# Kernel tuning notes

Measured on AMD Instinct MI355X. Metric: run time of the kernel, lower is better.

## Reference

```python
import jax, jax.numpy as jnp
import numpy as np

N_TRAIN = 16384
B_TEST = 4096
M_HALF = 768                 # modes per side -> M = 2*m+1 quadrature nodes
M_NODES = 2 * M_HALF + 1     # 1537
L_FFT = 4 * M_HALF + 1       # circulant embedding length (= 2*M-1)
H_SPACING = 0.01
SIGMASQ = 0.1
ELL = 0.1                    # SE kernel lengthscale
PROBES = 64
STEPS = 50
CG_ITERS = 50
TWO_PI = 2.0 * np.pi
EVAL_FLOOR = 1e-18


def setup_inputs():
    key = jax.random.key(0)
    k1, k2, k3, k4 = jax.random.split(key, 4)
    x = jax.random.uniform(k1, (N_TRAIN, 1), dtype=jnp.float32)
    y = jax.random.normal(k2, (N_TRAIN,), dtype=jnp.float32)
    x_new = jax.random.uniform(k3, (B_TEST, 1), dtype=jnp.float32)
    z = jax.random.normal(k4, (PROBES, M_NODES), dtype=jnp.float32)
    return {"x": x, "y": y, "x_new": x_new, "z": z}


def _cg(Aop, b, iters):
    """Conjugate gradients on Hermitian PD system, fixed iteration count."""
    x0 = jnp.zeros_like(b)
    rs0 = jnp.real(jnp.vdot(b, b))
    def step(carry, _):
        xk, rk, pk, rs = carry
        Ap = Aop(pk)
        a = (rs / jnp.real(jnp.vdot(pk, Ap))).astype(b.dtype)
        xk = xk + a * pk
        rk = rk - a * Ap
        rs_new = jnp.real(jnp.vdot(rk, rk))
        pk = rk + (rs_new / rs).astype(b.dtype) * pk
        return (xk, rk, pk, rs_new), None
    (xk, _, _, _), _ = jax.lax.scan(step, (x0, b, b, rs0), None, length=iters)
    return xk


def _efgp_forward(x, y, x_new, z):
    m = M_HALF
    ks = jnp.arange(-m, m + 1, dtype=jnp.float32)           # (M,)
    xis = H_SPACING * ks
    # squared-exponential spectral density, unit variance
    S = np.sqrt(TWO_PI) * ELL * jnp.exp(-2.0 * (np.pi * ELL * xis) ** 2)
    ws = jnp.sqrt(H_SPACING * S).astype(jnp.complex64)      # (M,) quadrature weights

    xf = x[:, 0]
    # convolution vector v[p] = sum_n exp(2*pi*i*h*p*x_n), p in [-2m, 2m]
    ps = jnp.arange(-2 * m, 2 * m + 1, dtype=jnp.float32)   # (L,)
    phase_v = (TWO_PI * H_SPACING) * jnp.outer(xf, ps)      # (N, L)
    vfull = jnp.exp(1j * phase_v).sum(axis=0)               # (L,) complex64
    # circulant first column c[q] = t[q] = v[-q]; T[j,k] = v[k-j]
    c = jnp.roll(vfull[::-1], 2 * m + 1)
    c_fft = jnp.fft.fft(c)

    def toeplitz(u):  # u: (..., M) complex -> (..., M)
        pad = jnp.zeros(u.shape[:-1] + (L_FFT - M_NODES,), u.dtype)
        upad = jnp.concatenate([u, pad], axis=-1)
        return jnp.fft.ifft(jnp.fft.fft(upad, axis=-1) * c_fft, axis=-1)[..., :M_NODES]

    # Fourier feature matrix F[n,k] = exp(2*pi*i*h*k*x_n)
    F = jnp.exp(1j * (TWO_PI * H_SPACING) * jnp.outer(xf, ks))  # (N, M)
    yc = y.astype(jnp.complex64)
    rhs = ws * (F.conj().T @ yc)                                 # ws * F^H y

    def A_mean(beta):  # ws T ws beta + sigma^2 beta
        return ws * toeplitz(ws * beta) + SIGMASQ * beta

    beta = _cg(A_mean, rhs, CG_ITERS)

    Fn = jnp.exp(1j * (TWO_PI * H_SPACING) * jnp.outer(x_new[:, 0], ks))  # (B, M)
    mean = jnp.real(Fn @ (ws * beta))                                      # (B,)

    # ---- stochastic Lanczos quadrature log-det of I + sigma^-2 D T D ----
    def Av(v):
        return v + (1.0 / SIGMASQ) * (ws * toeplitz(ws * v))

    zr = jnp.sign(z).astype(jnp.complex64)  # Rademacher probes (P, M)

    def lanczos(z1):
        nz2 = jnp.real(jnp.vdot(z1, z1))
        q0 = z1 / jnp.sqrt(nz2)
        def step(carry, _):
            q, q_prev, beta_prev = carry
            v = Av(q) - beta_prev * q_prev
            alpha = jnp.real(jnp.vdot(q, v))
            v = v - alpha * q
            beta = jnp.sqrt(jnp.real(jnp.vdot(v, v)))
            q_new = v / jnp.maximum(beta, 1e-12)
            return (q_new, q, beta), (alpha, beta)
        init = (q0, jnp.zeros_like(q0), jnp.zeros((), jnp.float32))
        _, (alphas, betas) = jax.lax.scan(step, init, None, length=STEPS)
        return alphas, betas, nz2

    alphas, betas, nz2 = jax.vmap(lanczos)(zr)  # (P, STEPS)

    def tridiag(a, b):
        return jnp.diag(a) + jnp.diag(b[:-1], 1) + jnp.diag(b[:-1], -1)

    Ts = jax.vmap(tridiag)(alphas, betas)       # (P, STEPS, STEPS)
    evals, evecs = jnp.linalg.eigh(Ts)
    evals = jnp.maximum(evals, EVAL_FLOOR)
    w1 = evecs[:, 0, :]                         # first component of each Ritz vector
    quad = jnp.sum(w1 ** 2 * jnp.log(evals), axis=-1) * nz2  # (P,)
    logdet = jnp.mean(quad) + N_TRAIN * np.log(SIGMASQ)

    alpha_vec = jnp.real(yc - F @ (ws * beta)) / SIGMASQ
    lml = -0.5 * jnp.dot(y, alpha_vec) - 0.5 * logdet \
          - 0.5 * N_TRAIN * np.log(2.0 * np.pi)
    return mean, lml


def reference(x, y, x_new, z):
    return _efgp_forward(x, y, x_new, z)
```

## Files before the change

kernel.cpp:

```cpp
#include <hip/hip_runtime.h>
#include <hip/hip_cooperative_groups.h>
#include <math.h>

namespace cg = cooperative_groups;

#define MN 1537
#define NFFT 4096
#define FBN (NFFT + NFFT/8 + NFFT/64)
#define CW 0.06283185307179587f
#define W4096 1.5339807878856412e-3f

__device__ __forceinline__ float2 cmulf(float2 a, float2 b) {
    return make_float2(a.x*b.x - a.y*b.y, a.x*b.y + a.y*b.x);
}
__device__ __forceinline__ float2 cadd(float2 a, float2 b){ return make_float2(a.x+b.x, a.y+b.y); }
__device__ __forceinline__ float2 csub(float2 a, float2 b){ return make_float2(a.x-b.x, a.y-b.y); }
__device__ __forceinline__ float2 mulnegi(float2 z){ return make_float2(z.y, -z.x); }
__device__ __forceinline__ float2 mulposi(float2 z){ return make_float2(-z.y, z.x); }
__device__ __forceinline__ float2 cconj(float2 z){ return make_float2(z.x, -z.y); }
__device__ __forceinline__ int PHI(int i){ return i + (i >> 3) + (i >> 6); }

__device__ __forceinline__ float ws_at(int k) {
    float xi = 0.01f * (float)(k - 768);
    float t  = 0.31415926535897931f * xi;
    float S  = 0.25066282746310002f * expf(-2.0f * t * t);
    return sqrtf(0.01f * S);
}

struct Tw { float2 w1, w2, w4, c1, c3; };

__device__ __forceinline__ Tw make_tw(float ang){
    Tw t;
    __sincosf(ang, &t.w1.y, &t.w1.x);
    t.w2 = cmulf(t.w1, t.w1);
    t.w4 = cmulf(t.w2, t.w2);
    const float R = 0.70710678118654752f;
    t.c1 = cmulf(t.w1, make_float2( R, -R));
    t.c3 = cmulf(t.w1, make_float2(-R, -R));
    return t;
}

template<int S>
__device__ __forceinline__ void fwd8c(float2* fb, int tt, const Tw& w){
    const int Q = 1 << (S-2);
    const int p = tt & (Q-1);
    const int g = tt >> (S-2);
    const int base = (g << (S+1)) + p;
    float2 a0 = fb[PHI(base      )], a1 = fb[PHI(base +   Q)];
    float2 a2 = fb[PHI(base + 2*Q)], a3 = fb[PHI(base + 3*Q)];
    float2 a4 = fb[PHI(base + 4*Q)], a5 = fb[PHI(base + 5*Q)];
    float2 a6 = fb[PHI(base + 6*Q)], a7 = fb[PHI(base + 7*Q)];
    float2 b0 = cadd(a0,a4), b1 = cadd(a1,a5), b2 = cadd(a2,a6), b3 = cadd(a3,a7);
    float2 b4 = cmulf(csub(a0,a4), w.w1);
    float2 b5 = cmulf(csub(a1,a5), w.c1);
    float2 b6 = mulnegi(cmulf(csub(a2,a6), w.w1));
    float2 b7 = cmulf(csub(a3,a7), w.c3);
    float2 c0 = cadd(b0,b2), c2 = cmulf(csub(b0,b2), w.w2);
    float2 c1 = cadd(b1,b3), c3 = mulnegi(cmulf(csub(b1,b3), w.w2));
    float2 c4 = cadd(b4,b6), c6 = cmulf(csub(b4,b6), w.w2);
    float2 c5 = cadd(b5,b7), c7 = mulnegi(cmulf(csub(b5,b7), w.w2));
    fb[PHI(base      )] = cadd(c0,c1);
    fb[PHI(base +   Q)] = cmulf(csub(c0,c1), w.w4);
    fb[PHI(base + 2*Q)] = cadd(c2,c3);
    fb[PHI(base + 3*Q)] = cmulf(csub(c2,c3), w.w4);
    fb[PHI(base + 4*Q)] = cadd(c4,c5);
    fb[PHI(base + 5*Q)] = cmulf(csub(c4,c5), w.w4);
    fb[PHI(base + 6*Q)] = cadd(c6,c7);
    fb[PHI(base + 7*Q)] = cmulf(csub(c6,c7), w.w4);
}

template<int S>
__device__ __forceinline__ void inv8c(float2* fb, int tt, const Tw& w){
    const int Q = 1 << S;
    const int p = tt & (Q-1);
    const int g = tt >> S;
    const int base = (g << (S+3)) + p;
    float2 u1 = cconj(w.w1), u2 = cconj(w.w2), u4 = cconj(w.w4);
    float2 uc1 = cconj(w.c1), uc3 = cconj(w.c3);
    float2 a0 = fb[PHI(base      )], a1 = fb[PHI(base +   Q)];
    float2 a2 = fb[PHI(base + 2*Q)], a3 = fb[PHI(base + 3*Q)];
    float2 a4 = fb[PHI(base + 4*Q)], a5 = fb[PHI(base + 5*Q)];
    float2 a6 = fb[PHI(base + 6*Q)], a7 = fb[PHI(base + 7*Q)];
    float2 m;
    m = cmulf(a1, u4); float2 t0 = cadd(a0,m), t1 = csub(a0,m);
    m = cmulf(a3, u4); float2 t2 = cadd(a2,m), t3 = csub(a2,m);
    m = cmulf(a5, u4); float2 t4 = cadd(a4,m), t5 = csub(a4,m);
    m = cmulf(a7, u4); float2 t6 = cadd(a6,m), t7 = csub(a6,m);
    m = cmulf(t2, u2);          float2 e0 = cadd(t0,m), e2 = csub(t0,m);
    m = mulposi(cmulf(t3, u2)); float2 e1 = cadd(t1,m), e3 = csub(t1,m);
    m = cmulf(t6, u2);          float2 e4 = cadd(t4,m), e6 = csub(t4,m);
    m = mulposi(cmulf(t7, u2)); float2 e5 = cadd(t5,m), e7 = csub(t5,m);
    m = cmulf(e4, u1);          fb[PHI(base      )] = cadd(e0,m); fb[PHI(base + 4*Q)] = csub(e0,m);
    m = cmulf(e5, uc1);         fb[PHI(base +   Q)] = cadd(e1,m); fb[PHI(base + 5*Q)] = csub(e1,m);
    m = mulposi(cmulf(e6, u1)); fb[PHI(base + 2*Q)] = cadd(e2,m); fb[PHI(base + 6*Q)] = csub(e2,m);
    m = cmulf(e7, uc3);         fb[PHI(base + 3*Q)] = cadd(e3,m); fb[PHI(base + 7*Q)] = csub(e3,m);
}

__device__ __forceinline__ void fwd8_first(float2* fb, int tt, const Tw& w, const float2* in){
    float2 b0 = in[0], b1 = in[1], b2 = in[2], b3 = in[3];
    float2 b4 = cmulf(in[0], w.w1);
    float2 b5 = cmulf(in[1], w.c1);
    float2 b6 = mulnegi(cmulf(in[2], w.w1));
    float2 b7 = cmulf(in[3], w.c3);
    float2 c0 = cadd(b0,b2), c2 = cmulf(csub(b0,b2), w.w2);
    float2 c1 = cadd(b1,b3), c3 = mulnegi(cmulf(csub(b1,b3), w.w2));
    float2 c4 = cadd(b4,b6), c6 = cmulf(csub(b4,b6), w.w2);
    float2 c5 = cadd(b5,b7), c7 = mulnegi(cmulf(csub(b5,b7), w.w2));
    fb[PHI(tt       )] = cadd(c0,c1);
    fb[PHI(tt +  512)] = cmulf(csub(c0,c1), w.w4);
    fb[PHI(tt + 1024)] = cadd(c2,c3);
    fb[PHI(tt + 1536)] = cmulf(csub(c2,c3), w.w4);
    fb[PHI(tt + 2048)] = cadd(c4,c5);
    fb[PHI(tt + 2560)] = cmulf(csub(c4,c5), w.w4);
    fb[PHI(tt + 3072)] = cadd(c6,c7);
    fb[PHI(tt + 3584)] = cmulf(csub(c6,c7), w.w4);
}

__device__ __forceinline__ void inv8_last(const float2* fb, int tt, const Tw& w, float2* outv){
    float2 u1 = cconj(w.w1), u2 = cconj(w.w2), u4 = cconj(w.w4);
    float2 uc1 = cconj(w.c1), uc3 = cconj(w.c3);
    float2 a0 = fb[PHI(tt       )], a1 = fb[PHI(tt +  512)];
    float2 a2 = fb[PHI(tt + 1024)], a3 = fb[PHI(tt + 1536)];
    float2 a4 = fb[PHI(tt + 2048)], a5 = fb[PHI(tt + 2560)];
    float2 a6 = fb[PHI(tt + 3072)], a7 = fb[PHI(tt + 3584)];
    float2 m;
    m = cmulf(a1, u4); float2 t0 = cadd(a0,m), t1 = csub(a0,m);
    m = cmulf(a3, u4); float2 t2 = cadd(a2,m), t3 = csub(a2,m);
    m = cmulf(a5, u4); float2 t4 = cadd(a4,m), t5 = csub(a4,m);
    m = cmulf(a7, u4); float2 t6 = cadd(a6,m), t7 = csub(a6,m);
    m = cmulf(t2, u2);          float2 e0 = cadd(t0,m), e2 = csub(t0,m);
    m = mulposi(cmulf(t3, u2)); float2 e1 = cadd(t1,m), e3 = csub(t1,m);
    m = cmulf(t6, u2);          float2 e4 = cadd(t4,m), e6 = csub(t4,m);
    m = mulposi(cmulf(t7, u2)); float2 e5 = cadd(t5,m), e7 = csub(t5,m);
    outv[0] = cadd(e0, cmulf(e4, u1));
    outv[1] = cadd(e1, cmulf(e5, uc1));
    outv[2] = cadd(e2, mulposi(cmulf(e6, u1)));
    outv[3] = cadd(e3, cmulf(e7, uc3));
}

__device__ __forceinline__ void mid8(float2* fb, int tt, const float2* g){
    const float R = 0.70710678118654752f;
    const int base = tt << 3;
    float2 a0 = fb[PHI(base  )], a1 = fb[PHI(base+1)];
    float2 a2 = fb[PHI(base+2)], a3 = fb[PHI(base+3)];
    float2 a4 = fb[PHI(base+4)], a5 = fb[PHI(base+5)];
    float2 a6 = fb[PHI(base+6)], a7 = fb[PHI(base+7)];
    float2 b0 = cadd(a0,a4), b1 = cadd(a1,a5), b2 = cadd(a2,a6), b3 = cadd(a3,a7);
    float2 b4 = csub(a0,a4);
    float2 b5 = cmulf(csub(a1,a5), make_float2( R, -R));
    float2 b6 = mulnegi(csub(a2,a6));
    float2 b7 = cmulf(csub(a3,a7), make_float2(-R, -R));
    float2 c0 = cadd(b0,b2), c2 = csub(b0,b2);
    float2 c1 = cadd(b1,b3), c3 = mulnegi(csub(b1,b3));
    float2 c4 = cadd(b4,b6), c6 = csub(b4,b6);
    float2 c5 = cadd(b5,b7), c7 = mulnegi(csub(b5,b7));
    float2 d0 = cadd(c0,c1), d1 = csub(c0,c1);
    float2 d2 = cadd(c2,c3), d3 = csub(c2,c3);
    float2 d4 = cadd(c4,c5), d5 = csub(c4,c5);
    float2 d6 = cadd(c6,c7), d7 = csub(c6,c7);
    d0 = cmulf(d0, g[0]); d1 = cmulf(d1, g[1]); d2 = cmulf(d2, g[2]); d3 = cmulf(d3, g[3]);
    d4 = cmulf(d4, g[4]); d5 = cmulf(d5, g[5]); d6 = cmulf(d6, g[6]); d7 = cmulf(d7, g[7]);
    float2 m;
    m = d1; float2 t0 = cadd(d0,m), t1 = csub(d0,m);
    m = d3; float2 t2 = cadd(d2,m), t3 = csub(d2,m);
    m = d5; float2 t4 = cadd(d4,m), t5 = csub(d4,m);
    m = d7; float2 t6 = cadd(d6,m), t7 = csub(d6,m);
    m = t2;          float2 e0 = cadd(t0,m), e2 = csub(t0,m);
    m = mulposi(t3); float2 e1 = cadd(t1,m), e3 = csub(t1,m);
    m = t6;          float2 e4 = cadd(t4,m), e6 = csub(t4,m);
    m = mulposi(t7); float2 e5 = cadd(t5,m), e7 = csub(t5,m);
    m = e4;                           fb[PHI(base  )] = cadd(e0,m); fb[PHI(base+4)] = csub(e0,m);
    m = cmulf(e5, make_float2(R, R)); fb[PHI(base+1)] = cadd(e1,m); fb[PHI(base+5)] = csub(e1,m);
    m = mulposi(e6);                  fb[PHI(base+2)] = cadd(e2,m); fb[PHI(base+6)] = csub(e2,m);
    m = cmulf(e7, make_float2(-R, R));fb[PHI(base+3)] = cadd(e3,m); fb[PHI(base+7)] = csub(e3,m);
}

__device__ __forceinline__ void fwd8_last_reg(const float2* fb, int tt, float2* gout){
    const float R = 0.70710678118654752f;
    const int base = tt << 3;
    float2 a0 = fb[PHI(base  )], a1 = fb[PHI(base+1)];
    float2 a2 = fb[PHI(base+2)], a3 = fb[PHI(base+3)];
    float2 a4 = fb[PHI(base+4)], a5 = fb[PHI(base+5)];
    float2 a6 = fb[PHI(base+6)], a7 = fb[PHI(base+7)];
    float2 b0 = cadd(a0,a4), b1 = cadd(a1,a5), b2 = cadd(a2,a6), b3 = cadd(a3,a7);
    float2 b4 = csub(a0,a4);
    float2 b5 = cmulf(csub(a1,a5), make_float2( R, -R));
    float2 b6 = mulnegi(csub(a2,a6));
    float2 b7 = cmulf(csub(a3,a7), make_float2(-R, -R));
    float2 c0 = cadd(b0,b2), c2 = csub(b0,b2);
    float2 c1 = cadd(b1,b3), c3 = mulnegi(csub(b1,b3));
    float2 c4 = cadd(b4,b6), c6 = csub(b4,b6);
    float2 c5 = cadd(b5,b7), c7 = mulnegi(csub(b5,b7));
    gout[0] = cadd(c0,c1); gout[1] = csub(c0,c1);
    gout[2] = cadd(c2,c3); gout[3] = csub(c2,c3);
    gout[4] = cadd(c4,c5); gout[5] = csub(c4,c5);
    gout[6] = cadd(c6,c7); gout[7] = csub(c6,c7);
}

__device__ __forceinline__ void conv_fft(float2* fb, const float2* g, int tid,
                                         const Tw& T11, const Tw& T8, const Tw& T5,
                                         const float2* in, float2* outv){
    __syncthreads();
    fwd8_first(fb, tid, T11, in); __syncthreads();
    fwd8c<8>(fb, tid, T8); __syncthreads();
    fwd8c<5>(fb, tid, T5); __syncthreads();
    mid8(fb, tid, g);      __syncthreads();
    inv8c<3>(fb, tid, T5); __syncthreads();
    inv8c<6>(fb, tid, T8); __syncthreads();
    inv8_last(fb, tid, T11, outv);
}

__device__ float block_reduce8(float v, volatile float* sc) {
    int lane = threadIdx.x & 63, wid = threadIdx.x >> 6;
    #pragma unroll
    for (int off = 32; off > 0; off >>= 1) v += __shfl_down(v, off, 64);
    if (lane == 0) sc[wid] = v;
    __syncthreads();
    if (wid == 0) {
        float s = (lane < 8) ? sc[lane] : 0.0f;
        #pragma unroll
        for (int off = 4; off > 0; off >>= 1) s += __shfl_down(s, off, 64);
        if (lane == 0) sc[16] = s;
    }
    __syncthreads();
    return sc[16];
}

__device__ float2 block_reduce2(float2 v, volatile float* sc) {
    int lane = threadIdx.x & 63, wid = threadIdx.x >> 6;
    #pragma unroll
    for (int off = 32; off > 0; off >>= 1) {
        v.x += __shfl_down(v.x, off, 64);
        v.y += __shfl_down(v.y, off, 64);
    }
    if (lane == 0) { sc[wid] = v.x; sc[17 + wid] = v.y; }
    __syncthreads();
    if (wid == 0) {
        float sx = (lane < 8) ? sc[lane] : 0.0f;
        float sy = (lane < 8) ? sc[17 + lane] : 0.0f;
        #pragma unroll
        for (int off = 4; off > 0; off >>= 1) {
            sx += __shfl_down(sx, off, 64);
            sy += __shfl_down(sy, off, 64);
        }
        if (lane == 0) { sc[16] = sx; sc[33] = sy; }
    }
    __syncthreads();
    return make_float2(sc[16], sc[33]);
}

__global__ __launch_bounds__(512) __attribute__((amdgpu_waves_per_eu(2, 2)))
void mega(const float* __restrict__ x, const float* __restrict__ y,
          const float* __restrict__ xn, const float* __restrict__ z,
          float* __restrict__ out,
          float2* __restrict__ d_v, float2* __restrict__ d_rhs, float2* __restrict__ d_wb,
          float* __restrict__ d_al, float* __restrict__ d_be, float* __restrict__ d_nz2,
          float* __restrict__ d_quad, float* __restrict__ d_t1p)
{
    __shared__ float2 fb[FBN];
    __shared__ float  redb[40];
    cg::grid_group grid = cg::this_grid();
    const int b = blockIdx.x, tid = threadIdx.x;
    const int wid = tid >> 6, lane = tid & 63;

    for (int c = b*8 + wid; c < 3073 + MN; c += 2048) {
        bool is_v = c < 3073;
        float pk = is_v ? (float)(c - 1536) : (float)(c - 3073 - 768);
        float sx = 0.f, sy = 0.f;
        if (is_v){
            for (int j = 0; j < 256; ++j){
                float ph = CW * (x[j*64 + lane] * pk);
                float s, cc; __sincosf(ph, &s, &cc);
                sx += cc; sy += s;
            }
        } else {
            for (int j = 0; j < 256; ++j){
                int n = j*64 + lane;
                float yv = y[n];
                float ph = CW * (x[n] * pk);
                float s, cc; __sincosf(ph, &s, &cc);
                sx += cc*yv; sy -= s*yv;
            }
        }
        #pragma unroll
        for (int off = 32; off > 0; off >>= 1){
            sx += __shfl_down(sx, off, 64);
            sy += __shfl_down(sy, off, 64);
        }
        if (lane == 0){
            if (is_v) d_v[c] = make_float2(sx, sy);
            else      d_rhs[c - 3073] = make_float2(sx, sy);
        }
    }
    grid.sync();

    if (b < 65) {
        Tw T11 = make_tw(-W4096 * (float)tid);
        Tw T8  = make_tw(-W4096 * (float)((tid & 63) << 3));
        Tw T5  = make_tw(-W4096 * (float)((tid & 7)  << 6));
        bool on3 = (tid == 0);
        float w[4];
        w[0] = ws_at(tid); w[1] = ws_at(tid + 512); w[2] = ws_at(tid + 1024);
        w[3] = on3 ? ws_at(1536) : 0.f;

        float2 g[8];
        #pragma unroll
        for (int k = 0; k < 8; ++k){
            int i = tid + k*512;
            float2 val = make_float2(0.f, 0.f);
            if (i == 0)            val = d_v[1536];
            else if (i <= 1536)    val = d_v[1536 - i];
            else if (i >= 2560)    val = d_v[5632 - i];
            fb[PHI(i)] = val;
        }
        __syncthreads();
        fwd8c<11>(fb, tid, T11); __syncthreads();
        fwd8c<8 >(fb, tid, T8);  __syncthreads();
        fwd8c<5 >(fb, tid, T5);  __syncthreads();
        fwd8_last_reg(fb, tid, g);

        float2 sin_[4], cv[4];
        if (b < 64) {
            float2 q[4], qp[4];
            float part = 0.f;
            #pragma unroll
            for (int s = 0; s < 4; ++s){
                float sv = 0.f;
                if (s < 3 || on3){
                    float zv = z[b*MN + tid + s*512];
                    sv = (zv > 0.f) ? 1.f : ((zv < 0.f) ? -1.f : 0.f);
                }
                q[s] = make_float2(sv, 0.f);
                qp[s] = make_float2(0.f, 0.f);
                part += sv * sv;
            }
            float nz2 = block_reduce8(part, redb);
            if (tid == 0) d_nz2[b] = nz2;
            float qs = 1.0f / sqrtf(nz2);
            #pragma unroll
            for (int s = 0; s < 4; ++s){ q[s].x *= qs; q[s].y *= qs; }
            float bp = 0.f;
            float cf[4];
            #pragma unroll
            for (int s = 0; s < 4; ++s) cf[s] = w[s] * (10.0f / 4096.0f);
            for (int step = 0; step < 50; ++step) {
                #pragma unroll
                for (int s = 0; s < 4; ++s)
                    sin_[s] = make_float2(w[s]*q[s].x, w[s]*q[s].y);
                conv_fft(fb, g, tid, T11, T8, T5, sin_, cv);
                float2 v[4];
                float2 pp = make_float2(0.f, 0.f);
                #pragma unroll
                for (int s = 0; s < 4; ++s){
                    v[s] = make_float2(q[s].x + cf[s]*cv[s].x - bp*qp[s].x,
                                       q[s].y + cf[s]*cv[s].y - bp*qp[s].y);
                    pp.x += q[s].x*v[s].x + q[s].y*v[s].y;
                    pp.y += v[s].x*v[s].x + v[s].y*v[s].y;
                }
                float2 rr = block_reduce2(pp, redb);
                float alpha = rr.x;
                float beta = sqrtf(fmaxf(rr.y - alpha*alpha, 0.f));
                if (tid == 0) { d_al[b*50 + step] = alpha; d_be[b*50 + step] = beta; }
                float binv = 1.0f / fmaxf(beta, 1e-12f);
                #pragma unroll
                for (int s = 0; s < 4; ++s){
                    float2 nq = make_float2((v[s].x - alpha*q[s].x)*binv,
                                            (v[s].y - alpha*q[s].y)*binv);
                    qp[s] = q[s];
                    q[s] = nq;
                }
                bp = beta;
            }
        } else {
            float2 r[4], p[4], xx[4];
            float part = 0.f;
            #pragma unroll
            for (int s = 0; s < 4; ++s){
                float2 bj = make_float2(0.f, 0.f);
                if (s < 3 || on3){
                    float2 rv = d_rhs[tid + s*512];
                    bj = make_float2(w[s]*rv.x, w[s]*rv.y);
                }
                r[s] = bj; p[s] = bj; xx[s] = make_float2(0.f, 0.f);
                part += bj.x*bj.x + bj.y*bj.y;
            }
            float rs = block_reduce8(part, redb);
            float cf[4];
            #pragma unroll
            for (int s = 0; s < 4; ++s) cf[s] = w[s] * (1.0f / 4096.0f);
            for (int it = 0; it < 50; ++it) {
                #pragma unroll
                for (int s = 0; s < 4; ++s)
                    sin_[s] = make_float2(w[s]*p[s].x, w[s]*p[s].y);
                conv_fft(fb, g, tid, T11, T8, T5, sin_, cv);
                float2 ap[4];
                part = 0.f;
                #pragma unroll
                for (int s = 0; s < 4; ++s){
                    ap[s] = make_float2(cf[s]*cv[s].x + 0.1f*p[s].x,
                                        cf[s]*cv[s].y + 0.1f*p[s].y);
                    part += p[s].x*ap[s].x + p[s].y*ap[s].y;
                }
                float pAp = block_reduce8(part, redb);
                float a = rs / pAp;
                part = 0.f;
                #pragma unroll
                for (int s = 0; s < 4; ++s){
                    xx[s].x += a*p[s].x; xx[s].y += a*p[s].y;
                    r[s].x -= a*ap[s].x; r[s].y -= a*ap[s].y;
                    part += r[s].x*r[s].x + r[s].y*r[s].y;
                }
                float rsn = block_reduce8(part, redb);
                float sc = rsn / rs;
                #pragma unroll
                for (int s = 0; s < 4; ++s)
                    p[s] = make_float2(r[s].x + sc*p[s].x, r[s].y + sc*p[s].y);
                rs = rsn;
            }
            #pragma unroll
            for (int s = 0; s < 4; ++s){
                if (s < 3 || on3)
                    d_wb[tid + s*512] = make_float2(w[s]*xx[s].x, w[s]*xx[s].y);
            }
        }
    }
    grid.sync();

    if (b < 64) {
        if (tid < 64) {
            float* sa  = (float*)fb;
            float* se  = sa + 64;
            float* se2 = sa + 128;
            int t = tid;
            if (t < 50) {
                sa[t] = d_al[b*50 + t];
                float bv = (t < 49) ? d_be[b*50 + t] : 0.0f;
                se[t] = bv; se2[t] = bv * bv;
            }
            float quad = 0.0f;
            if (t < 50) {
                float lo = 3.4e38f, hi = -3.4e38f;
                for (int i = 0; i < 50; ++i) {
                    float rr = ((i > 0) ? fabsf(se[i-1]) : 0.0f) + ((i < 49) ? fabsf(se[i]) : 0.0f);
                    lo = fminf(lo, sa[i] - rr);
                    hi = fmaxf(hi, sa[i] + rr);
                }
                for (int it = 0; it < 38; ++it) {
                    float mid = 0.5f * (lo + hi);
                    int cnt = 0;
                    float qq = sa[0] - mid;
                    cnt += (qq < 0.0f);
                    for (int k = 1; k < 50; ++k) {
                        float dnm = (fabsf(qq) < 1e-30f) ? ((qq < 0.0f) ? -1e-30f : 1e-30f) : qq;
                        qq = (sa[k] - mid) - se2[k-1] * __builtin_amdgcn_rcpf(dnm);
                        cnt += (qq < 0.0f);
                    }
                    if (cnt > t) hi = mid; else lo = mid;
                }
                float lam = 0.5f * (lo + hi);
                float pm = 0.0f, pc = 1.0f, s = 1.0f, bprev = 0.0f;
                for (int k = 0; k < 49; ++k) {
                    float bk = fmaxf(se[k], 1e-30f);
                    float pn = ((lam - sa[k]) * pc - bprev * pm) * __builtin_amdgcn_rcpf(bk);
                    pn = fminf(fmaxf(pn, -1e18f), 1e18f);
                    s += pn * pn;
                    pm = pc; pc = pn; bprev = bk;
                }
                quad = logf(fmaxf(lam, 1e-18f)) / s;
            }
            #pragma unroll
            for (int off = 32; off > 0; off >>= 1) quad += __shfl_down(quad, off, 64);
            if (t == 0) d_quad[b] = quad * d_nz2[b];
        }
    } else if (b < 96) {
        int row = (b - 64)*128 + (tid >> 2);
        int sub = tid & 3;
        float xv = xn[row];
        float acc = 0.f;
        for (int k = sub; k < MN; k += 4) {
            float ph = CW * (xv * (float)(k - 768));
            float s, c; __sincosf(ph, &s, &c);
            float2 ww = d_wb[k];
            acc += c * ww.x - s * ww.y;
        }
        acc += __shfl_down(acc, 2, 4);
        acc += __shfl_down(acc, 1, 4);
        if (sub == 0) out[row] = acc;
    } else if (b < 224) {
        int n = (b - 96)*128 + (tid >> 2);
        int sub = tid & 3;
        float xv = x[n], yv = y[n];
        float acc = 0.f;
        for (int k = sub; k < MN; k += 4) {
            float ph = CW * (xv * (float)(k - 768));
            float s, c; __sincosf(ph, &s, &c);
            float2 ww = d_wb[k];
            acc += c * ww.x - s * ww.y;
        }
        acc += __shfl_down(acc, 2, 4);
        acc += __shfl_down(acc, 1, 4);
        float contrib = (sub == 0) ? yv * (yv - acc) * 10.0f : 0.f;
        #pragma unroll
        for (int off = 32; off > 0; off >>= 1) contrib += __shfl_down(contrib, off, 64);
        if (lane == 0) redb[wid] = contrib;
        __syncthreads();
        if (tid == 0) {
            float s = 0.f;
            #pragma unroll
            for (int i = 0; i < 8; ++i) s += redb[i];
            d_t1p[b - 96] = s;
        }
    }
    grid.sync();

    if (b == 0 && tid < 64) {
        float qv = d_quad[tid];
        float t1 = d_t1p[tid] + d_t1p[tid + 64];
        #pragma unroll
        for (int off = 32; off > 0; off >>= 1) {
            qv += __shfl_down(qv, off, 64);
            t1 += __shfl_down(t1, off, 64);
        }
        if (tid == 0) {
            float ld = qv / 64.0f - 37725.5542f;
            out[4096] = -0.5f * t1 - 0.5f * ld - 15055.8889f;
        }
    }
}

extern "C" void kernel_launch(void* const* d_in, const int* in_sizes, int n_in,
                              void* d_out, int out_size, void* d_ws, size_t ws_size,
                              hipStream_t stream) {
    const float* d_x  = (const float*)d_in[0];
    const float* d_y  = (const float*)d_in[1];
    const float* d_xn = (const float*)d_in[2];
    const float* d_z  = (const float*)d_in[3];
    float* out = (float*)d_out;
    char* w = (char*)d_ws;
    float2* d_v   = (float2*)(w + 0);
    float2* d_rhs = (float2*)(w + 24832);
    float2* d_wb  = (float2*)(w + 37376);
    float*  d_al  = (float*)(w + 49920);
    float*  d_be  = (float*)(w + 62720);
    float*  d_nz2 = (float*)(w + 75520);
    float*  d_quad= (float*)(w + 75776);
    float*  d_t1p = (float*)(w + 76032);

    void* args[] = { (void*)&d_x, (void*)&d_y, (void*)&d_xn, (void*)&d_z, (void*)&out,
                     (void*)&d_v, (void*)&d_rhs, (void*)&d_wb, (void*)&d_al, (void*)&d_be,
                     (void*)&d_nz2, (void*)&d_quad, (void*)&d_t1p };
    hipLaunchCooperativeKernel((const void*)mega, dim3(256), dim3(512), args, 0, stream);
}
```

Baseline: 477.6 us.

## Pack two Lanczos probes per 1024-thread block with XOR-swizzled FFT shared memory

The cooperative grid drops from 256 blocks of 512 threads to 64 blocks of 1024, with each block running two independent probe FFT/Lanczos pipelines in halves that use separate shared-memory buffers. The padded PHI indexing becomes an XOR swizzle. Block reductions reuse the FFT buffer, and the mean and data-fit evaluation is redistributed as one wavefront per row, with an atomicAdd accumulator replacing partial sums. This aims to cut grid-sync cost and idle blocks. In exchange, the two halves share one __syncthreads barrier, so they advance together, and there are fewer blocks in total, which lowers overall parallelism for the Lanczos and CG phase.

```diff
diff --git a/kernel.cpp b/kernel.cpp
--- a/kernel.cpp
+++ b/kernel.cpp
@@ -6,7 +6,6 @@
 
 #define MN 1537
 #define NFFT 4096
-#define FBN (NFFT + NFFT/8 + NFFT/64)
 #define CW 0.06283185307179587f
 #define W4096 1.5339807878856412e-3f
 
@@ -18,7 +17,7 @@
 __device__ __forceinline__ float2 mulnegi(float2 z){ return make_float2(z.y, -z.x); }
 __device__ __forceinline__ float2 mulposi(float2 z){ return make_float2(-z.y, z.x); }
 __device__ __forceinline__ float2 cconj(float2 z){ return make_float2(z.x, -z.y); }
-__device__ __forceinline__ int PHI(int i){ return i + (i >> 3) + (i >> 6); }
+__device__ __forceinline__ int SW(int i){ return i ^ ((i >> 3) & 15); }
 
 __device__ __forceinline__ float ws_at(int k) {
     float xi = 0.01f * (float)(k - 768);
@@ -46,10 +45,10 @@
     const int p = tt & (Q-1);
     const int g = tt >> (S-2);
     const int base = (g << (S+1)) + p;
-    float2 a0 = fb[PHI(base      )], a1 = fb[PHI(base +   Q)];
-    float2 a2 = fb[PHI(base + 2*Q)], a3 = fb[PHI(base + 3*Q)];
-    float2 a4 = fb[PHI(base + 4*Q)], a5 = fb[PHI(base + 5*Q)];
-    float2 a6 = fb[PHI(base + 6*Q)], a7 = fb[PHI(base + 7*Q)];
+    float2 a0 = fb[SW(base      )], a1 = fb[SW(base +   Q)];
+    float2 a2 = fb[SW(base + 2*Q)], a3 = fb[SW(base + 3*Q)];
+    float2 a4 = fb[SW(base + 4*Q)], a5 = fb[SW(base + 5*Q)];
+    float2 a6 = fb[SW(base + 6*Q)], a7 = fb[SW(base + 7*Q)];
     float2 b0 = cadd(a0,a4), b1 = cadd(a1,a5), b2 = cadd(a2,a6), b3 = cadd(a3,a7);
     float2 b4 = cmulf(csub(a0,a4), w.w1);
     float2 b5 = cmulf(csub(a1,a5), w.c1);
@@ -59,14 +58,14 @@
     float2 c1 = cadd(b1,b3), c3 = mulnegi(cmulf(csub(b1,b3), w.w2));
     float2 c4 = cadd(b4,b6), c6 = cmulf(csub(b4,b6), w.w2);
     float2 c5 = cadd(b5,b7), c7 = mulnegi(cmulf(csub(b5,b7), w.w2));
-    fb[PHI(base      )] = cadd(c0,c1);
-    fb[PHI(base +   Q)] = cmulf(csub(c0,c1), w.w4);
-    fb[PHI(base + 2*Q)] = cadd(c2,c3);
-    fb[PHI(base + 3*Q)] = cmulf(csub(c2,c3), w.w4);
-    fb[PHI(base + 4*Q)] = cadd(c4,c5);
-    fb[PHI(base + 5*Q)] = cmulf(csub(c4,c5), w.w4);
-    fb[PHI(base + 6*Q)] = cadd(c6,c7);
-    fb[PHI(base + 7*Q)] = cmulf(csub(c6,c7), w.w4);
+    fb[SW(base      )] = cadd(c0,c1);
+    fb[SW(base +   Q)] = cmulf(csub(c0,c1), w.w4);
+    fb[SW(base + 2*Q)] = cadd(c2,c3);
+    fb[SW(base + 3*Q)] = cmulf(csub(c2,c3), w.w4);
+    fb[SW(base + 4*Q)] = cadd(c4,c5);
+    fb[SW(base + 5*Q)] = cmulf(csub(c4,c5), w.w4);
+    fb[SW(base + 6*Q)] = cadd(c6,c7);
+    fb[SW(base + 7*Q)] = cmulf(csub(c6,c7), w.w4);
 }
 
 template<int S>
@@ -77,10 +76,10 @@
     const int base = (g << (S+3)) + p;
     float2 u1 = cconj(w.w1), u2 = cconj(w.w2), u4 = cconj(w.w4);
     float2 uc1 = cconj(w.c1), uc3 = cconj(w.c3);
-    float2 a0 = fb[PHI(base      )], a1 = fb[PHI(base +   Q)];
-    float2 a2 = fb[PHI(base + 2*Q)], a3 = fb[PHI(base + 3*Q)];
-    float2 a4 = fb[PHI(base + 4*Q)], a5 = fb[PHI(base + 5*Q)];
-    float2 a6 = fb[PHI(base + 6*Q)], a7 = fb[PHI(base + 7*Q)];
+    float2 a0 = fb[SW(base      )], a1 = fb[SW(base +   Q)];
+    float2 a2 = fb[SW(base + 2*Q)], a3 = fb[SW(base + 3*Q)];
+    float2 a4 = fb[SW(base + 4*Q)], a5 = fb[SW(base + 5*Q)];
+    float2 a6 = fb[SW(base + 6*Q)], a7 = fb[SW(base + 7*Q)];
     float2 m;
     m = cmulf(a1, u4); float2 t0 = cadd(a0,m), t1 = csub(a0,m);
     m = cmulf(a3, u4); float2 t2 = cadd(a2,m), t3 = csub(a2,m);
@@ -90,10 +89,10 @@
     m = mulposi(cmulf(t3, u2)); float2 e1 = cadd(t1,m), e3 = csub(t1,m);
     m = cmulf(t6, u2);          float2 e4 = cadd(t4,m), e6 = csub(t4,m);
     m = mulposi(cmulf(t7, u2)); float2 e5 = cadd(t5,m), e7 = csub(t5,m);
-    m = cmulf(e4, u1);          fb[PHI(base      )] = cadd(e0,m); fb[PHI(base + 4*Q)] = csub(e0,m);
-    m = cmulf(e5, uc1);         fb[PHI(base +   Q)] = cadd(e1,m); fb[PHI(base + 5*Q)] = csub(e1,m);
-    m = mulposi(cmulf(e6, u1)); fb[PHI(base + 2*Q)] = cadd(e2,m); fb[PHI(base + 6*Q)] = csub(e2,m);
-    m = cmulf(e7, uc3);         fb[PHI(base + 3*Q)] = cadd(e3,m); fb[PHI(base + 7*Q)] = csub(e3,m);
+    m = cmulf(e4, u1);          fb[SW(base      )] = cadd(e0,m); fb[SW(base + 4*Q)] = csub(e0,m);
+    m = cmulf(e5, uc1);         fb[SW(base +   Q)] = cadd(e1,m); fb[SW(base + 5*Q)] = csub(e1,m);
+    m = mulposi(cmulf(e6, u1)); fb[SW(base + 2*Q)] = cadd(e2,m); fb[SW(base + 6*Q)] = csub(e2,m);
+    m = cmulf(e7, uc3);         fb[SW(base + 3*Q)] = cadd(e3,m); fb[SW(base + 7*Q)] = csub(e3,m);
 }
 
 __device__ __forceinline__ void fwd8_first(float2* fb, int tt, const Tw& w, const float2* in){
@@ -106,23 +105,23 @@
     float2 c1 = cadd(b1,b3), c3 = mulnegi(cmulf(csub(b1,b3), w.w2));
     float2 c4 = cadd(b4,b6), c6 = cmulf(csub(b4,b6), w.w2);
     float2 c5 = cadd(b5,b7), c7 = mulnegi(cmulf(csub(b5,b7), w.w2));
-    fb[PHI(tt       )] = cadd(c0,c1);
-    fb[PHI(tt +  512)] = cmulf(csub(c0,c1), w.w4);
-    fb[PHI(tt + 1024)] = cadd(c2,c3);
-    fb[PHI(tt + 1536)] = cmulf(csub(c2,c3), w.w4);
-    fb[PHI(tt + 2048)] = cadd(c4,c5);
-    fb[PHI(tt + 2560)] = cmulf(csub(c4,c5), w.w4);
-    fb[PHI(tt + 3072)] = cadd(c6,c7);
-    fb[PHI(tt + 3584)] = cmulf(csub(c6,c7), w.w4);
+    fb[SW(tt       )] = cadd(c0,c1);
+    fb[SW(tt +  512)] = cmulf(csub(c0,c1), w.w4);
+    fb[SW(tt + 1024)] = cadd(c2,c3);
+    fb[SW(tt + 1536)] = cmulf(csub(c2,c3), w.w4);
+    fb[SW(tt + 2048)] = cadd(c4,c5);
+    fb[SW(tt + 2560)] = cmulf(csub(c4,c5), w.w4);
+    fb[SW(tt + 3072)] = cadd(c6,c7);
+    fb[SW(tt + 3584)] = cmulf(csub(c6,c7), w.w4);
 }
 
 __device__ __forceinline__ void inv8_last(const float2* fb, int tt, const Tw& w, float2* outv){
     float2 u1 = cconj(w.w1), u2 = cconj(w.w2), u4 = cconj(w.w4);
     float2 uc1 = cconj(w.c1), uc3 = cconj(w.c3);
-    float2 a0 = fb[PHI(tt       )], a1 = fb[PHI(tt +  512)];
-    float2 a2 = fb[PHI(tt + 1024)], a3 = fb[PHI(tt + 1536)];
-    float2 a4 = fb[PHI(tt + 2048)], a5 = fb[PHI(tt + 2560)];
-    float2 a6 = fb[PHI(tt + 3072)], a7 = fb[PHI(tt + 3584)];
+    float2 a0 = fb[SW(tt       )], a1 = fb[SW(tt +  512)];
+    float2 a2 = fb[SW(tt + 1024)], a3 = fb[SW(tt + 1536)];
+    float2 a4 = fb[SW(tt + 2048)], a5 = fb[SW(tt + 2560)];
+    float2 a6 = fb[SW(tt + 3072)], a7 = fb[SW(tt + 3584)];
     float2 m;
     m = cmulf(a1, u4); float2 t0 = cadd(a0,m), t1 = csub(a0,m);
     m = cmulf(a3, u4); float2 t2 = cadd(a2,m), t3 = csub(a2,m);
@@ -141,10 +140,10 @@
 __device__ __forceinline__ void mid8(float2* fb, int tt, const float2* g){
     const float R = 0.70710678118654752f;
     const int base = tt << 3;
-    float2 a0 = fb[PHI(base  )], a1 = fb[PHI(base+1)];
-    float2 a2 = fb[PHI(base+2)], a3 = fb[PHI(base+3)];
-    float2 a4 = fb[PHI(base+4)], a5 = fb[PHI(base+5)];
-    float2 a6 = fb[PHI(base+6)], a7 = fb[PHI(base+7)];
+    float2 a0 = fb[SW(base  )], a1 = fb[SW(base+1)];
+    float2 a2 = fb[SW(base+2)], a3 = fb[SW(base+3)];
+    float2 a4 = fb[SW(base+4)], a5 = fb[SW(base+5)];
+    float2 a6 = fb[SW(base+6)], a7 = fb[SW(base+7)];
     float2 b0 = cadd(a0,a4), b1 = cadd(a1,a5), b2 = cadd(a2,a6), b3 = cadd(a3,a7);
     float2 b4 = csub(a0,a4);
     float2 b5 = cmulf(csub(a1,a5), make_float2( R, -R));
@@ -169,19 +168,19 @@
     m = mulposi(t3); float2 e1 = cadd(t1,m), e3 = csub(t1,m);
     m = t6;          float2 e4 = cadd(t4,m), e6 = csub(t4,m);
     m = mulposi(t7); float2 e5 = cadd(t5,m), e7 = csub(t5,m);
-    m = e4;                           fb[PHI(base  )] = cadd(e0,m); fb[PHI(base+4)] = csub(e0,m);
-    m = cmulf(e5, make_float2(R, R)); fb[PHI(base+1)] = cadd(e1,m); fb[PHI(base+5)] = csub(e1,m);
-    m = mulposi(e6);                  fb[PHI(base+2)] = cadd(e2,m); fb[PHI(base+6)] = csub(e2,m);
-    m = cmulf(e7, make_float2(-R, R));fb[PHI(base+3)] = cadd(e3,m); fb[PHI(base+7)] = csub(e3,m);
+    m = e4;                           fb[SW(base  )] = cadd(e0,m); fb[SW(base+4)] = csub(e0,m);
+    m = cmulf(e5, make_float2(R, R)); fb[SW(base+1)] = cadd(e1,m); fb[SW(base+5)] = csub(e1,m);
+    m = mulposi(e6);                  fb[SW(base+2)] = cadd(e2,m); fb[SW(base+6)] = csub(e2,m);
+    m = cmulf(e7, make_float2(-R, R));fb[SW(base+3)] = cadd(e3,m); fb[SW(base+7)] = csub(e3,m);
 }
 
 __device__ __forceinline__ void fwd8_last_reg(const float2* fb, int tt, float2* gout){
     const float R = 0.70710678118654752f;
     const int base = tt << 3;
-    float2 a0 = fb[PHI(base  )], a1 = fb[PHI(base+1)];
-    float2 a2 = fb[PHI(base+2)], a3 = fb[PHI(base+3)];
-    float2 a4 = fb[PHI(base+4)], a5 = fb[PHI(base+5)];
-    float2 a6 = fb[PHI(base+6)], a7 = fb[PHI(base+7)];
+    float2 a0 = fb[SW(base  )], a1 = fb[SW(base+1)];
+    float2 a2 = fb[SW(base+2)], a3 = fb[SW(base+3)];
+    float2 a4 = fb[SW(base+4)], a5 = fb[SW(base+5)];
+    float2 a6 = fb[SW(base+6)], a7 = fb[SW(base+7)];
     float2 b0 = cadd(a0,a4), b1 = cadd(a1,a5), b2 = cadd(a2,a6), b3 = cadd(a3,a7);
     float2 b4 = csub(a0,a4);
     float2 b5 = cmulf(csub(a1,a5), make_float2( R, -R));
@@ -197,73 +196,56 @@
     gout[6] = cadd(c6,c7); gout[7] = csub(c6,c7);
 }
 
-__device__ __forceinline__ void conv_fft(float2* fb, const float2* g, int tid,
+__device__ __forceinline__ void conv_fft(float2* fb, const float2* g, int tt,
                                          const Tw& T11, const Tw& T8, const Tw& T5,
                                          const float2* in, float2* outv){
     __syncthreads();
-    fwd8_first(fb, tid, T11, in); __syncthreads();
-    fwd8c<8>(fb, tid, T8); __syncthreads();
-    fwd8c<5>(fb, tid, T5); __syncthreads();
-    mid8(fb, tid, g);      __syncthreads();
-    inv8c<3>(fb, tid, T5); __syncthreads();
-    inv8c<6>(fb, tid, T8); __syncthreads();
-    inv8_last(fb, tid, T11, outv);
-}
-
-__device__ float block_reduce8(float v, volatile float* sc) {
-    int lane = threadIdx.x & 63, wid = threadIdx.x >> 6;
+    fwd8_first(fb, tt, T11, in); __syncthreads();
+    fwd8c<8>(fb, tt, T8); __syncthreads();
+    fwd8c<5>(fb, tt, T5); __syncthreads();
+    mid8(fb, tt, g);      __syncthreads();
+    inv8c<3>(fb, tt, T5); __syncthreads();
+    inv8c<6>(fb, tt, T8); __syncthreads();
+    inv8_last(fb, tt, T11, outv);
+}
+
+__device__ __forceinline__ float2 hreduce2(float2 v, float2* fbh, int tt){
+    int lane = tt & 63, w8 = tt >> 6;
     #pragma unroll
-    for (int off = 32; off > 0; off >>= 1) v += __shfl_down(v, off, 64);
-    if (lane == 0) sc[wid] = v;
-    __syncthreads();
-    if (wid == 0) {
-        float s = (lane < 8) ? sc[lane] : 0.0f;
-        #pragma unroll
-        for (int off = 4; off > 0; off >>= 1) s += __shfl_down(s, off, 64);
-        if (lane == 0) sc[16] = s;
-    }
-    __syncthreads();
-    return sc[16];
-}
-
-__device__ float2 block_reduce2(float2 v, volatile float* sc) {
-    int lane = threadIdx.x & 63, wid = threadIdx.x >> 6;
-    #pragma unroll
-    for (int off = 32; off > 0; off >>= 1) {
+    for (int off = 32; off > 0; off >>= 1){
         v.x += __shfl_down(v.x, off, 64);
         v.y += __shfl_down(v.y, off, 64);
     }
-    if (lane == 0) { sc[wid] = v.x; sc[17 + wid] = v.y; }
+    if (lane == 0) fbh[SW(64*w8)] = v;
     __syncthreads();
-    if (wid == 0) {
-        float sx = (lane < 8) ? sc[lane] : 0.0f;
-        float sy = (lane < 8) ? sc[17 + lane] : 0.0f;
+    if (w8 == 0){
+        float2 s = (lane < 8) ? fbh[SW(64*lane)] : make_float2(0.f, 0.f);
         #pragma unroll
-        for (int off = 4; off > 0; off >>= 1) {
-            sx += __shfl_down(sx, off, 64);
-            sy += __shfl_down(sy, off, 64);
-        }
-        if (lane == 0) { sc[16] = sx; sc[33] = sy; }
+        for (int off = 4; off > 0; off >>= 1){
+            s.x += __shfl_down(s.x, off, 64);
+            s.y += __shfl_down(s.y, off, 64);
+        }
+        if (lane == 0) fbh[0] = s;
     }
     __syncthreads();
-    return make_float2(sc[16], sc[33]);
-}
-
-__global__ __launch_bounds__(512) __attribute__((amdgpu_waves_per_eu(2, 2)))
+    return fbh[0];
+}
+
+__global__ __launch_bounds__(1024)
 void mega(const float* __restrict__ x, const float* __restrict__ y,
           const float* __restrict__ xn, const float* __restrict__ z,
           float* __restrict__ out,
           float2* __restrict__ d_v, float2* __restrict__ d_rhs, float2* __restrict__ d_wb,
           float* __restrict__ d_al, float* __restrict__ d_be, float* __restrict__ d_nz2,
-          float* __restrict__ d_quad, float* __restrict__ d_t1p)
+          float* __restrict__ d_quad, float* __restrict__ d_t1)
 {
-    __shared__ float2 fb[FBN];
-    __shared__ float  redb[40];
+    __shared__ float2 fb2[2][NFFT];
     cg::grid_group grid = cg::this_grid();
     const int b = blockIdx.x, tid = threadIdx.x;
     const int wid = tid >> 6, lane = tid & 63;
 
-    for (int c = b*8 + wid; c < 3073 + MN; c += 2048) {
+    if (b == 0 && tid == 0) *d_t1 = 0.f;
+    for (int c = b*16 + wid; c < 3073 + MN; c += 1024) {
         bool is_v = c < 3073;
         float pk = is_v ? (float)(c - 1536) : (float)(c - 3073 - 768);
         float sx = 0.f, sy = 0.f;
@@ -294,48 +276,53 @@
     }
     grid.sync();
 
-    if (b < 65) {
-        Tw T11 = make_tw(-W4096 * (float)tid);
-        Tw T8  = make_tw(-W4096 * (float)((tid & 63) << 3));
-        Tw T5  = make_tw(-W4096 * (float)((tid & 7)  << 6));
-        bool on3 = (tid == 0);
+    if (b < 33) {
+        const int h = tid >> 9;
+        const int tt = tid & 511;
+        float2* fbh = fb2[h];
+        Tw T11 = make_tw(-W4096 * (float)tt);
+        Tw T8  = make_tw(-W4096 * (float)((tt & 63) << 3));
+        Tw T5  = make_tw(-W4096 * (float)((tt & 7)  << 6));
+        bool on3 = (tt == 0);
         float w[4];
-        w[0] = ws_at(tid); w[1] = ws_at(tid + 512); w[2] = ws_at(tid + 1024);
+        w[0] = ws_at(tt); w[1] = ws_at(tt + 512); w[2] = ws_at(tt + 1024);
         w[3] = on3 ? ws_at(1536) : 0.f;
 
         float2 g[8];
         #pragma unroll
         for (int k = 0; k < 8; ++k){
-            int i = tid + k*512;
+            int i = tt + k*512;
             float2 val = make_float2(0.f, 0.f);
             if (i == 0)            val = d_v[1536];
             else if (i <= 1536)    val = d_v[1536 - i];
             else if (i >= 2560)    val = d_v[5632 - i];
-            fb[PHI(i)] = val;
+            fbh[SW(i)] = val;
         }
         __syncthreads();
-        fwd8c<11>(fb, tid, T11); __syncthreads();
-        fwd8c<8 >(fb, tid, T8);  __syncthreads();
-        fwd8c<5 >(fb, tid, T5);  __syncthreads();
-        fwd8_last_reg(fb, tid, g);
+        fwd8c<11>(fbh, tt, T11); __syncthreads();
+        fwd8c<8 >(fbh, tt, T8);  __syncthreads();
+        fwd8c<5 >(fbh, tt, T5);  __syncthreads();
+        fwd8_last_reg(fbh, tt, g);
+        __syncthreads();
 
         float2 sin_[4], cv[4];
-        if (b < 64) {
+        if (b < 32) {
+            const int probe = 2*b + h;
             float2 q[4], qp[4];
             float part = 0.f;
             #pragma unroll
             for (int s = 0; s < 4; ++s){
                 float sv = 0.f;
                 if (s < 3 || on3){
-                    float zv = z[b*MN + tid + s*512];
+                    float zv = z[probe*MN + tt + s*512];
                     sv = (zv > 0.f) ? 1.f : ((zv < 0.f) ? -1.f : 0.f);
                 }
                 q[s] = make_float2(sv, 0.f);
                 qp[s] = make_float2(0.f, 0.f);
                 part += sv * sv;
             }
-            float nz2 = block_reduce8(part, redb);
-            if (tid == 0) d_nz2[b] = nz2;
+            float nz2 = hreduce2(make_float2(part, 0.f), fbh, tt).x;
+            if (tt == 0) d_nz2[probe] = nz2;
             float qs = 1.0f / sqrtf(nz2);
             #pragma unroll
             for (int s = 0; s < 4; ++s){ q[s].x *= qs; q[s].y *= qs; }
@@ -347,7 +334,7 @@
                 #pragma unroll
                 for (int s = 0; s < 4; ++s)
                     sin_[s] = make_float2(w[s]*q[s].x, w[s]*q[s].y);
-                conv_fft(fb, g, tid, T11, T8, T5, sin_, cv);
+                conv_fft(fbh, g, tt, T11, T8, T5, sin_, cv);
                 float2 v[4];
                 float2 pp = make_float2(0.f, 0.f);
                 #pragma unroll
@@ -357,10 +344,10 @@
                     pp.x += q[s].x*v[s].x + q[s].y*v[s].y;
                     pp.y += v[s].x*v[s].x + v[s].y*v[s].y;
                 }
-                float2 rr = block_reduce2(pp, redb);
+                float2 rr = hreduce2(pp, fbh, tt);
                 float alpha = rr.x;
                 float beta = sqrtf(fmaxf(rr.y - alpha*alpha, 0.f));
-                if (tid == 0) { d_al[b*50 + step] = alpha; d_be[b*50 + step] = beta; }
+                if (tt == 0) { d_al[probe*50 + step] = alpha; d_be[probe*50 + step] = beta; }
                 float binv = 1.0f / fmaxf(beta, 1e-12f);
                 #pragma unroll
                 for (int s = 0; s < 4; ++s){
@@ -378,13 +365,13 @@
             for (int s = 0; s < 4; ++s){
                 float2 bj = make_float2(0.f, 0.f);
                 if (s < 3 || on3){
-                    float2 rv = d_rhs[tid + s*512];
+                    float2 rv = d_rhs[tt + s*512];
                     bj = make_float2(w[s]*rv.x, w[s]*rv.y);
                 }
                 r[s] = bj; p[s] = bj; xx[s] = make_float2(0.f, 0.f);
                 part += bj.x*bj.x + bj.y*bj.y;
             }
-            float rs = block_reduce8(part, redb);
+            float rs = hreduce2(make_float2(part, 0.f), fbh, tt).x;
             float cf[4];
             #pragma unroll
             for (int s = 0; s < 4; ++s) cf[s] = w[s] * (1.0f / 4096.0f);
@@ -392,7 +379,7 @@
                 #pragma unroll
                 for (int s = 0; s < 4; ++s)
                     sin_[s] = make_float2(w[s]*p[s].x, w[s]*p[s].y);
-                conv_fft(fb, g, tid, T11, T8, T5, sin_, cv);
+                conv_fft(fbh, g, tt, T11, T8, T5, sin_, cv);
                 float2 ap[4];
                 part = 0.f;
                 #pragma unroll
@@ -401,7 +388,7 @@
                                         cf[s]*cv[s].y + 0.1f*p[s].y);
                     part += p[s].x*ap[s].x + p[s].y*ap[s].y;
                 }
-                float pAp = block_reduce8(part, redb);
+                float pAp = hreduce2(make_float2(part, 0.f), fbh, tt).x;
                 float a = rs / pAp;
                 part = 0.f;
                 #pragma unroll
@@ -410,120 +397,99 @@
                     r[s].x -= a*ap[s].x; r[s].y -= a*ap[s].y;
                     part += r[s].x*r[s].x + r[s].y*r[s].y;
                 }
-                float rsn = block_reduce8(part, redb);
+                float rsn = hreduce2(make_float2(part, 0.f), fbh, tt).x;
                 float sc = rsn / rs;
                 #pragma unroll
                 for (int s = 0; s < 4; ++s)
                     p[s] = make_float2(r[s].x + sc*p[s].x, r[s].y + sc*p[s].y);
                 rs = rsn;
             }
-            #pragma unroll
-            for (int s = 0; s < 4; ++s){
-                if (s < 3 || on3)
-                    d_wb[tid + s*512] = make_float2(w[s]*xx[s].x, w[s]*xx[s].y);
+            if (h == 0){
+                #pragma unroll
+                for (int s = 0; s < 4; ++s){
+                    if (s < 3 || on3)
+                        d_wb[tt + s*512] = make_float2(w[s]*xx[s].x, w[s]*xx[s].y);
+                }
             }
         }
     }
     grid.sync();
 
-    if (b < 64) {
-        if (tid < 64) {
-            float* sa  = (float*)fb;
-            float* se  = sa + 64;
-            float* se2 = sa + 128;
-            int t = tid;
-            if (t < 50) {
-                sa[t] = d_al[b*50 + t];
-                float bv = (t < 49) ? d_be[b*50 + t] : 0.0f;
-                se[t] = bv; se2[t] = bv * bv;
-            }
-            float quad = 0.0f;
-            if (t < 50) {
-                float lo = 3.4e38f, hi = -3.4e38f;
-                for (int i = 0; i < 50; ++i) {
-                    float rr = ((i > 0) ? fabsf(se[i-1]) : 0.0f) + ((i < 49) ? fabsf(se[i]) : 0.0f);
-                    lo = fminf(lo, sa[i] - rr);
-                    hi = fmaxf(hi, sa[i] + rr);
-                }
-                for (int it = 0; it < 38; ++it) {
-                    float mid = 0.5f * (lo + hi);
-                    int cnt = 0;
-                    float qq = sa[0] - mid;
+    if (wid == 0) {
+        float* sa  = (float*)(&fb2[0][0]);
+        float* se  = sa + 64;
+        float* se2 = sa + 128;
+        int t = lane;
+        if (t < 50) {
+            sa[t] = d_al[b*50 + t];
+            float bv = (t < 49) ? d_be[b*50 + t] : 0.0f;
+            se[t] = bv; se2[t] = bv * bv;
+        }
+        float quad = 0.0f;
+        if (t < 50) {
+            float lo = 3.4e38f, hi = -3.4e38f;
+            for (int i = 0; i < 50; ++i) {
+                float rr = ((i > 0) ? fabsf(se[i-1]) : 0.0f) + ((i < 49) ? fabsf(se[i]) : 0.0f);
+                lo = fminf(lo, sa[i] - rr);
+                hi = fmaxf(hi, sa[i] + rr);
+            }
+            for (int it = 0; it < 38; ++it) {
+                float mid = 0.5f * (lo + hi);
+                int cnt = 0;
+                float qq = sa[0] - mid;
+                cnt += (qq < 0.0f);
+                for (int k = 1; k < 50; ++k) {
+                    float dnm = (fabsf(qq) < 1e-30f) ? ((qq < 0.0f) ? -1e-30f : 1e-30f) : qq;
+                    qq = (sa[k] - mid) - se2[k-1] * __builtin_amdgcn_rcpf(dnm);
                     cnt += (qq < 0.0f);
-                    for (int k = 1; k < 50; ++k) {
-                        float dnm = (fabsf(qq) < 1e-30f) ? ((qq < 0.0f) ? -1e-30f : 1e-30f) : qq;
-                        qq = (sa[k] - mid) - se2[k-1] * __builtin_amdgcn_rcpf(dnm);
-                        cnt += (qq < 0.0f);
-                    }
-                    if (cnt > t) hi = mid; else lo = mid;
-                }
-                float lam = 0.5f * (lo + hi);
-                float pm = 0.0f, pc = 1.0f, s = 1.0f, bprev = 0.0f;
-                for (int k = 0; k < 49; ++k) {
-                    float bk = fmaxf(se[k], 1e-30f);
-                    float pn = ((lam - sa[k]) * pc - bprev * pm) * __builtin_amdgcn_rcpf(bk);
-                    pn = fminf(fmaxf(pn, -1e18f), 1e18f);
-                    s += pn * pn;
-                    pm = pc; pc = pn; bprev = bk;
-                }
-                quad = logf(fmaxf(lam, 1e-18f)) / s;
+                }
+                if (cnt > t) hi = mid; else lo = mid;
+            }
+            float lam = 0.5f * (lo + hi);
+            float pm = 0.0f, pc = 1.0f, s = 1.0f, bprev = 0.0f;
+            for (int k = 0; k < 49; ++k) {
+                float bk = fmaxf(se[k], 1e-30f);
+                float pn = ((lam - sa[k]) * pc - bprev * pm) * __builtin_amdgcn_rcpf(bk);
+                pn = fminf(fmaxf(pn, -1e18f), 1e18f);
+                s += pn * pn;
+                pm = pc; pc = pn; bprev = bk;
+            }
+            quad = logf(fmaxf(lam, 1e-18f)) / s;
+        }
+        #pragma unroll
+        for (int off = 32; off > 0; off >>= 1) quad += __shfl_down(quad, off, 64);
+        if (t == 0) d_quad[b] = quad * d_nz2[b];
+    } else {
+        float ta = 0.f;
+        for (int r = b*15 + (wid - 1); r < 4096 + 16384; r += 960) {
+            bool ismean = r < 4096;
+            int n = ismean ? r : (r - 4096);
+            float xv = ismean ? xn[n] : x[n];
+            float acc = 0.f;
+            for (int k = lane; k < MN; k += 64) {
+                float ph = CW * (xv * (float)(k - 768));
+                float s, c; __sincosf(ph, &s, &c);
+                float2 ww = d_wb[k];
+                acc += c * ww.x - s * ww.y;
             }
             #pragma unroll
-            for (int off = 32; off > 0; off >>= 1) quad += __shfl_down(quad, off, 64);
-            if (t == 0) d_quad[b] = quad * d_nz2[b];
-        }
-    } else if (b < 96) {
-        int row = (b - 64)*128 + (tid >> 2);
-        int sub = tid & 3;
-        float xv = xn[row];
-        float acc = 0.f;
-        for (int k = sub; k < MN; k += 4) {
-            float ph = CW * (xv * (float)(k - 768));
-            float s, c; __sincosf(ph, &s, &c);
-            float2 ww = d_wb[k];
-            acc += c * ww.x - s * ww.y;
-        }
-        acc += __shfl_down(acc, 2, 4);
-        acc += __shfl_down(acc, 1, 4);
-        if (sub == 0) out[row] = acc;
-    } else if (b < 224) {
-        int n = (b - 96)*128 + (tid >> 2);
-        int sub = tid & 3;
-        float xv = x[n], yv = y[n];
-        float acc = 0.f;
-        for (int k = sub; k < MN; k += 4) {
-            float ph = CW * (xv * (float)(k - 768));
-            float s, c; __sincosf(ph, &s, &c);
-            float2 ww = d_wb[k];
-            acc += c * ww.x - s * ww.y;
-        }
-        acc += __shfl_down(acc, 2, 4);
-        acc += __shfl_down(acc, 1, 4);
-        float contrib = (sub == 0) ? yv * (yv - acc) * 10.0f : 0.f;
-        #pragma unroll
-        for (int off = 32; off > 0; off >>= 1) contrib += __shfl_down(contrib, off, 64);
-        if (lane == 0) redb[wid] = contrib;
-        __syncthreads();
-        if (tid == 0) {
-            float s = 0.f;
-            #pragma unroll
-            for (int i = 0; i < 8; ++i) s += redb[i];
-            d_t1p[b - 96] = s;
-        }
+            for (int off = 32; off > 0; off >>= 1) acc += __shfl_down(acc, off, 64);
+            if (lane == 0) {
+                if (ismean) out[n] = acc;
+                else { float yv = y[n]; ta += yv * (yv - acc) * 10.0f; }
+            }
+        }
+        if (lane == 0) atomicAdd(d_t1, ta);
     }
     grid.sync();
 
     if (b == 0 && tid < 64) {
         float qv = d_quad[tid];
-        float t1 = d_t1p[tid] + d_t1p[tid + 64];
         #pragma unroll
-        for (int off = 32; off > 0; off >>= 1) {
-            qv += __shfl_down(qv, off, 64);
-            t1 += __shfl_down(t1, off, 64);
-        }
+        for (int off = 32; off > 0; off >>= 1) qv += __shfl_down(qv, off, 64);
         if (tid == 0) {
             float ld = qv / 64.0f - 37725.5542f;
-            out[4096] = -0.5f * t1 - 0.5f * ld - 15055.8889f;
+            out[4096] = -0.5f * (*d_t1) - 0.5f * ld - 15055.8889f;
         }
     }
 }
@@ -544,10 +510,10 @@
     float*  d_be  = (float*)(w + 62720);
     float*  d_nz2 = (float*)(w + 75520);
     float*  d_quad= (float*)(w + 75776);
-    float*  d_t1p = (float*)(w + 76032);
+    float*  d_t1  = (float*)(w + 76032);
 
     void* args[] = { (void*)&d_x, (void*)&d_y, (void*)&d_xn, (void*)&d_z, (void*)&out,
                      (void*)&d_v, (void*)&d_rhs, (void*)&d_wb, (void*)&d_al, (void*)&d_be,
-                     (void*)&d_nz2, (void*)&d_quad, (void*)&d_t1p };
-    hipLaunchCooperativeKernel((const void*)mega, dim3(256), dim3(512), args, 0, stream);
-}
+                     (void*)&d_nz2, (void*)&d_quad, (void*)&d_t1 };
+    hipLaunchCooperativeKernel((const void*)mega, dim3(64), dim3(1024), args, 0, stream);
+}
```

After: 1.241 ms. 2.6x slower.
